# Kernel optimization log

Hardware: AMD Instinct MI355X
Metric: run time of the kernel (lower is better)

## Reference

```python
import jax, jax.numpy as jnp
import numpy as np


def _wn_dense_relu(x, v, g, bias):
    # torch weight_norm over dim=0: w[h,:] = g[h] * v[h,:] / ||v[h,:]||
    w = g[:, None] * v / jnp.linalg.norm(v, axis=1, keepdims=True)  # (hid, inp)
    return jax.nn.relu(jnp.einsum('bld,hd->blh', x, w) + bias)


def _masked_softmax(scores, mask, axis):
    # additive large-negative masking, numerically stable softmax
    return jax.nn.softmax(scores + jnp.where(mask > 0, 0.0, -1e9), axis=axis)


def setup_inputs() -> dict:
    key = jax.random.key(0)
    ks = jax.random.split(key, 6)
    B, La, Lb, D, H = 8, 2048, 2048, 256, 256
    return {
        'a': jax.random.normal(ks[0], (B, La, D), dtype=jnp.float32),
        'b': jax.random.normal(ks[1], (B, Lb, D), dtype=jnp.float32),
        'mask_a': jax.random.randint(ks[2], (B, La), 0, 2, dtype=jnp.int32),
        'mask_b': jax.random.randint(ks[3], (B, Lb), 0, 2, dtype=jnp.int32),
        'a_v': jax.random.normal(ks[4], (H, D), dtype=jnp.float32) * (2.0 / D) ** 0.5,
        'a_g': jnp.ones((H,), dtype=jnp.float32),
        'a_bias': jnp.zeros((H,), dtype=jnp.float32),
        'b_v': jax.random.normal(ks[5], (H, D), dtype=jnp.float32) * (2.0 / D) ** 0.5,
        'b_g': jnp.ones((H,), dtype=jnp.float32),
        'b_bias': jnp.zeros((H,), dtype=jnp.float32),
        'tau': jnp.asarray((1.0 / H) ** 0.5, dtype=jnp.float32),
    }


def reference(a, b, mask_a, mask_b, a_v, a_g, a_bias, b_v, b_g, b_bias, tau):
    ha = _wn_dense_relu(a, a_v, a_g, a_bias)                 # (B, La, H)
    hb = _wn_dense_relu(b, b_v, b_g, b_bias)                 # (B, Lb, H)
    attn = jnp.einsum('bih,bjh->bij', ha, hb) * tau          # (B, La, Lb)
    weight_a = _masked_softmax(attn, mask_a[:, :, None], axis=1)  # softmax over La
    weight_b = _masked_softmax(attn, mask_b[:, None, :], axis=2)  # softmax over Lb
    align_a = jnp.einsum('bij,bjd->bid', weight_b, b)        # (B, La, D)
    align_b = jnp.einsum('bij,bid->bjd', weight_a, a)        # (B, Lb, D)
    return align_a, align_b
```

## Files before the change

kernel.cpp:

```cpp
#include <hip/hip_runtime.h>
#include <hip/hip_bf16.h>
#include <stdint.h>

#define B_   8
#define L_   2048
#define D_   256
#define H_   256
#define TJ   64
#define NT   (L_/TJ)
#define BM   64
#define LOG2E 1.4426950408889634f

typedef short bf16x8 __attribute__((ext_vector_type(8)));
typedef short bf16x4 __attribute__((ext_vector_type(4)));
typedef unsigned short u16x4 __attribute__((ext_vector_type(4)));
typedef float f32x4  __attribute__((ext_vector_type(4)));

#define MFMA(a,b,c) __builtin_amdgcn_mfma_f32_16x16x32_bf16(a,b,c,0,0,0)
#define EX2(x) __builtin_amdgcn_exp2f(x)

typedef unsigned int u32;
__device__ __forceinline__ void gload_lds16(const void* g, void* l){
  __builtin_amdgcn_global_load_lds((const __attribute__((address_space(1))) u32*)g,
                                   (__attribute__((address_space(3))) u32*)l, 16, 0, 0);
}

__device__ __forceinline__ unsigned short f2bf(float f){
  __hip_bfloat16 h = __float2bfloat16(f);
  unsigned short us;
  __builtin_memcpy(&us, &h, 2);
  return us;
}
__device__ __forceinline__ float bf2f(unsigned short u){
  u32 t = ((u32)u) << 16;
  float f;
  __builtin_memcpy(&f, &t, 4);
  return f;
}

__device__ __forceinline__ void bar_lgkm(){
  asm volatile("s_waitcnt lgkmcnt(0)" ::: "memory");
  __builtin_amdgcn_s_barrier();
  __builtin_amdgcn_sched_barrier(0);
}
__device__ __forceinline__ void bar_all(){
  asm volatile("s_waitcnt vmcnt(0) lgkmcnt(0)" ::: "memory");
  __builtin_amdgcn_s_barrier();
  __builtin_amdgcn_sched_barrier(0);
}

__global__ __launch_bounds__(256) void wnorm_kernel(const float* __restrict__ av,
      const float* __restrict__ ag, const float* __restrict__ bv,
      const float* __restrict__ bg, unsigned short* __restrict__ wa,
      unsigned short* __restrict__ wb, float* __restrict__ maxn){
  int sel = blockIdx.y;
  if (blockIdx.x == 0 && threadIdx.x < 8) maxn[sel*8 + threadIdx.x] = 0.f;
  const float* v = sel ? bv : av;
  const float* g = sel ? bg : ag;
  unsigned short* w = sel ? wb : wa;
  int h = blockIdx.x;
  int d = threadIdx.x;
  float x = v[h*D_ + d];
  float sq = x*x;
  for (int off = 32; off; off >>= 1) sq += __shfl_down(sq, off, 64);
  __shared__ float red[4];
  int lane = threadIdx.x & 63, wid = threadIdx.x >> 6;
  if (lane == 0) red[wid] = sq;
  __syncthreads();
  float tot = red[0] + red[1] + red[2] + red[3];
  float scale = g[h] / sqrtf(tot);
  w[h*D_ + d] = f2bf(x * scale);
}

__global__ __launch_bounds__(256) void hgemm_kernel(const float* __restrict__ a,
      const float* __restrict__ b, const unsigned short* __restrict__ wa,
      const unsigned short* __restrict__ wb, const float* __restrict__ a_bias,
      const float* __restrict__ b_bias, const float* __restrict__ tau_ptr,
      unsigned short* __restrict__ ha, unsigned short* __restrict__ hb,
      unsigned short* __restrict__ aT, unsigned short* __restrict__ bT,
      float* __restrict__ rn_a, float* __restrict__ rn_b,
      float* __restrict__ maxn){
  __shared__ __align__(16) unsigned short xlk[64][256];
  __shared__ float redm[4];
  int sel = blockIdx.y;
  const float* x = sel ? b : a;
  const unsigned short* w = sel ? wb : wa;
  const float* bias = sel ? b_bias : a_bias;
  unsigned short* hx = sel ? hb : ha;
  unsigned short* xT = sel ? bT : aT;
  float* rn = sel ? rn_b : rn_a;
  float scale = sel ? 1.0f : tau_ptr[0] * LOG2E;
  int m0 = blockIdx.x * 64;
  int bz = m0 / L_, l0 = m0 % L_;
  int tid = threadIdx.x;
  int lane = tid & 63, wid = tid >> 6;
  int p = lane & 15, q = lane >> 4;

  {
    int r0 = tid >> 6;
    int c  = (tid & 63) * 4;
    int slot = c >> 3, half = (c >> 2) & 1;
    #pragma unroll
    for (int it = 0; it < 16; ++it){
      int row = it*4 + r0;
      f32x4 v = *(const f32x4*)(x + (size_t)(m0 + row) * 256 + c);
      uint2 wv;
      wv.x = (u32)f2bf(v[0]) | ((u32)f2bf(v[1]) << 16);
      wv.y = (u32)f2bf(v[2]) | ((u32)f2bf(v[3]) << 16);
      *(uint2*)((char*)&xlk[row][0] + ((slot ^ (row & 7)) << 4) + half*8) = wv;
    }
  }
  __syncthreads();

  bf16x8 af[8];
  {
    int row = wid*16 + p;
    #pragma unroll
    for (int kk = 0; kk < 8; ++kk)
      af[kk] = *(const bf16x8*)((char*)&xlk[row][0] + (((kk*4 + q) ^ (row & 7)) << 4));
  }
  f32x4 acc[16] = {};
  #pragma unroll
  for (int kk = 0; kk < 8; kk++){
    #pragma unroll
    for (int n = 0; n < 16; n++){
      bf16x8 bfr = *(const bf16x8*)(w + (size_t)(n*16 + p) * 256 + kk*32 + q*8);
      acc[n] = MFMA(af[kk], bfr, acc[n]);
    }
  }

  float rs[4] = {0.f, 0.f, 0.f, 0.f};
  #pragma unroll
  for (int n = 0; n < 16; n++){
    float bv = bias[n*16 + p];
    #pragma unroll
    for (int r = 0; r < 4; r++){
      int orow = m0 + wid*16 + q*4 + r;
      float vv = acc[n][r] + bv;
      vv = vv > 0.f ? vv : 0.f;
      float sv = vv * scale;
      rs[r] += sv * sv;
      hx[(size_t)orow * 256 + n*16 + p] = f2bf(sv);
    }
  }
  #pragma unroll
  for (int off = 1; off < 16; off <<= 1)
    #pragma unroll
    for (int r = 0; r < 4; r++)
      rs[r] += __shfl_xor(rs[r], off, 64);
  float lmax = 0.f;
  float rv[4];
  #pragma unroll
  for (int r = 0; r < 4; r++){
    rv[r] = sqrtf(rs[r]) * 1.01f;
    lmax = fmaxf(lmax, rv[r]);
  }
  if (p == 0){
    #pragma unroll
    for (int r = 0; r < 4; r++)
      rn[m0 + wid*16 + q*4 + r] = rv[r];
  }
  lmax = fmaxf(lmax, __shfl_xor(lmax, 16, 64));
  lmax = fmaxf(lmax, __shfl_xor(lmax, 32, 64));
  if (lane == 0) redm[wid] = lmax;
  __syncthreads();
  if (tid == 0){
    float bm = fmaxf(fmaxf(redm[0], redm[1]), fmaxf(redm[2], redm[3]));
    atomicMax((u32*)&maxn[sel*8 + bz], __float_as_uint(bm));
  }

  #pragma unroll
  for (int it = 0; it < 16; it++){
    int d = it*16 + (tid >> 4);
    int c = (tid & 15) * 4;
    bf16x4 v;
    #pragma unroll
    for (int j = 0; j < 4; j++){
      int row = c + j;
      v[j] = (short)*((const unsigned short*)((char*)&xlk[row][0]
                + (((d >> 3) ^ (row & 7)) << 4)) + (d & 7));
    }
    *(bf16x4*)(xT + ((size_t)bz*D_ + d)*L_ + l0 + c) = v;
  }
}

__global__ __launch_bounds__(256, 2) void flash_kernel(
    const unsigned short* __restrict__ ha, const unsigned short* __restrict__ hb,
    const unsigned short* __restrict__ aT, const unsigned short* __restrict__ bT,
    const int* __restrict__ mask_a, const int* __restrict__ mask_b,
    const float* __restrict__ rn_a, const float* __restrict__ rn_b,
    const float* __restrict__ maxn, float* __restrict__ out)
{
  __shared__ __align__(16) unsigned short HBT[64][256];
  __shared__ __align__(16) unsigned short VTL[256][64];
  __shared__ __align__(16) unsigned short WT[2][32][64];
  __shared__ unsigned short MSKB[2048];
  __shared__ float SST[4][32];

  const int bid = blockIdx.x;
  const int s   = bid & 15;
  const int dir = s >> 3;
  const int bz  = s & 7;
  const int i0  = (bid >> 4) * BM;
  const int tid = threadIdx.x;
  const int lane = tid & 63;
  const int wid  = tid >> 6;
  const int wr = wid >> 1, wc = wid & 1;
  const int p = lane & 15, q = lane >> 4;

  const unsigned short* hA = dir ? hb : ha;
  const unsigned short* hB = dir ? ha : hb;
  const unsigned short* vT = dir ? aT : bT;
  const int* mask = dir ? mask_a : mask_b;
  const float* rnA = dir ? rn_b : rn_a;
  const float mxB  = maxn[(dir ^ 1)*8 + bz];
  float* outp = out + ((size_t)dir * B_ + bz) * L_ * D_;

  const unsigned short* hAp = hA + (size_t)bz * L_ * H_;
  const unsigned short* hBp = hB + (size_t)bz * L_ * H_;
  const unsigned short* vTp = vT + (size_t)bz * D_ * L_;
  const int* mp = mask + bz * L_;

  const int hb_r0 = tid >> 5;
  const int hb_s  = tid & 31;
  const int vt_r0 = tid >> 3;
  const int vt_s  = tid & 7;

  bf16x8 af[2][8];
  #pragma unroll
  for (int g = 0; g < 2; ++g)
    #pragma unroll
    for (int kk = 0; kk < 8; ++kk)
      af[g][kk] = *(const bf16x8*)(hAp + (size_t)(i0 + wr*32 + g*16 + p) * H_ + kk*32 + q*8);

  float m_p[2];
  #pragma unroll
  for (int g = 0; g < 2; ++g)
    m_p[g] = rnA[bz*L_ + i0 + wr*32 + g*16 + p] * mxB;

  #pragma unroll
  for (int i = 0; i < 8; ++i){
    int idx = tid + i*256;
    MSKB[idx] = f2bf((mp[idx] > 0) ? 0.f : -1e9f);
  }

  f32x4 acc[2][8];
  #pragma unroll
  for (int g = 0; g < 2; ++g)
    #pragma unroll
    for (int n = 0; n < 8; ++n) acc[g][n] = (f32x4){0.f,0.f,0.f,0.f};
  float s_run[2];
  s_run[0] = s_run[1] = 0.f;

  #define STAGE_HB(jj0) do {                                                      \
    _Pragma("unroll")                                                             \
    for (int k = 0; k < 8; ++k){                                                  \
      int rr = k*8 + hb_r0;                                                       \
      int sp = hb_s ^ (rr & 7);                                                   \
      gload_lds16(hBp + (size_t)((jj0) + rr) * H_ + sp*8,                         \
                  &HBT[0][0] + k*2048 + tid*8);                                   \
    }                                                                             \
  } while(0)
  #define STAGE_VT(jj0) do {                                                      \
    _Pragma("unroll")                                                             \
    for (int k = 0; k < 8; ++k){                                                  \
      int rr = k*32 + vt_r0;                                                      \
      int sp = vt_s ^ (rr & 7);                                                   \
      gload_lds16(vTp + (size_t)rr * L_ + (jj0) + sp*8,                           \
                  &VTL[0][0] + k*2048 + tid*8);                                   \
    }                                                                             \
  } while(0)

  STAGE_HB(0);
  STAGE_VT(0);
  bar_all();

  for (int jt = 0; jt < NT; ++jt){
    const int j0 = jt * TJ;

    f32x4 accp[2][2];
    #pragma unroll
    for (int g = 0; g < 2; ++g)
      #pragma unroll
      for (int cg = 0; cg < 2; ++cg) accp[g][cg] = (f32x4){0.f,0.f,0.f,0.f};
    __builtin_amdgcn_s_setprio(1);
    #pragma unroll
    for (int kk = 0; kk < 8; ++kk){
      const int rb = wc*32 + p;
      const int sp = ((kk*4 + q) ^ (p & 7)) * 8;
      bf16x8 b0 = *(const bf16x8*)(&HBT[0][0] + rb*256 + sp);
      bf16x8 b1 = *(const bf16x8*)(&HBT[0][0] + (rb+16)*256 + sp);
      accp[0][0] = MFMA(b0, af[0][kk], accp[0][0]);
      accp[1][0] = MFMA(b0, af[1][kk], accp[1][0]);
      accp[0][1] = MFMA(b1, af[0][kk], accp[0][1]);
      accp[1][1] = MFMA(b1, af[1][kk], accp[1][1]);
    }
    __builtin_amdgcn_s_setprio(0);

    u16x4 k0 = *(const u16x4*)(&MSKB[j0 + wc*32 + q*4]);
    u16x4 k1 = *(const u16x4*)(&MSKB[j0 + wc*32 + 16 + q*4]);
    f32x4 mm0, mm1;
    #pragma unroll
    for (int r = 0; r < 4; ++r){ mm0[r] = bf2f(k0[r]); mm1[r] = bf2f(k1[r]); }

    #pragma unroll
    for (int g = 0; g < 2; ++g){
      #pragma unroll
      for (int cg = 0; cg < 2; ++cg){
        const f32x4 mm = cg ? mm1 : mm0;
        float w0 = EX2(accp[g][cg][0] + mm[0] - m_p[g]);
        float w1 = EX2(accp[g][cg][1] + mm[1] - m_p[g]);
        float w2 = EX2(accp[g][cg][2] + mm[2] - m_p[g]);
        float w3 = EX2(accp[g][cg][3] + mm[3] - m_p[g]);
        s_run[g] += (w0 + w1) + (w2 + w3);
        uint2 wv;
        wv.x = (u32)f2bf(w0) | ((u32)f2bf(w1) << 16);
        wv.y = (u32)f2bf(w2) | ((u32)f2bf(w3) << 16);
        int row = g*16 + p;
        int sl  = (wc*4 + cg*2 + (q>>1)) ^ (row & 7);
        *(uint2*)(&WT[wr][0][0] + row*64 + (sl<<3) + ((q&1)<<2)) = wv;
      }
    }
    bar_lgkm();

    if (jt + 1 < NT) STAGE_HB(j0 + TJ);

    bf16x8 wf[2][2];
    #pragma unroll
    for (int g = 0; g < 2; ++g)
      #pragma unroll
      for (int ks = 0; ks < 2; ++ks){
        int row = g*16 + p;
        wf[g][ks] = *(const bf16x8*)(&WT[wr][0][0] + row*64
                                     + ((((ks*4 + q) ^ (row & 7)))<<3));
      }

    __builtin_amdgcn_s_setprio(1);
    #pragma unroll
    for (int n = 0; n < 8; ++n){
      const int d = wc*128 + n*16 + p;
      #pragma unroll
      for (int ks = 0; ks < 2; ++ks){
        const int sp = ((ks*4 + q) ^ (d & 7)) * 8;
        bf16x8 vf = *(const bf16x8*)(&VTL[0][0] + d*64 + sp);
        acc[0][n] = MFMA(wf[0][ks], vf, acc[0][n]);
        acc[1][n] = MFMA(wf[1][ks], vf, acc[1][n]);
      }
    }
    __builtin_amdgcn_s_setprio(0);

    bar_all();
    if (jt + 1 < NT){
      STAGE_VT(j0 + TJ);
      bar_all();
    }
  }
  #undef STAGE_HB
  #undef STAGE_VT

  s_run[0] += __shfl_xor(s_run[0], 16, 64);
  s_run[0] += __shfl_xor(s_run[0], 32, 64);
  s_run[1] += __shfl_xor(s_run[1], 16, 64);
  s_run[1] += __shfl_xor(s_run[1], 32, 64);
  if (q == 0){
    SST[wid][p]      = s_run[0];
    SST[wid][16 + p] = s_run[1];
  }
  __syncthreads();
  float invS[2][4];
  #pragma unroll
  for (int g = 0; g < 2; ++g)
    #pragma unroll
    for (int r = 0; r < 4; ++r){
      int idx = g*16 + q*4 + r;
      invS[g][r] = 1.0f / (SST[wr*2][idx] + SST[wr*2 + 1][idx]);
    }

  #pragma unroll
  for (int g = 0; g < 2; ++g)
    #pragma unroll
    for (int n = 0; n < 8; ++n)
      #pragma unroll
      for (int r = 0; r < 4; ++r){
        int row = i0 + wr*32 + g*16 + q*4 + r;
        outp[(size_t)row * D_ + wc*128 + n*16 + p] = acc[g][n][r] * invS[g][r];
      }
}

extern "C" void kernel_launch(void* const* d_in, const int* in_sizes, int n_in,
                              void* d_out, int out_size, void* d_ws, size_t ws_size,
                              hipStream_t stream) {
  const float* a      = (const float*)d_in[0];
  const float* b      = (const float*)d_in[1];
  const int*   mask_a = (const int*)d_in[2];
  const int*   mask_b = (const int*)d_in[3];
  const float* a_v    = (const float*)d_in[4];
  const float* a_g    = (const float*)d_in[5];
  const float* a_bias = (const float*)d_in[6];
  const float* b_v    = (const float*)d_in[7];
  const float* b_g    = (const float*)d_in[8];
  const float* b_bias = (const float*)d_in[9];
  const float* tau    = (const float*)d_in[10];

  float* out = (float*)d_out;

  char* ws = (char*)d_ws;
  const size_t SZ_W  = (size_t)H_ * D_ * 2;
  const size_t SZ_H  = (size_t)B_ * L_ * H_ * 2;
  unsigned short* wa = (unsigned short*)(ws);
  unsigned short* wb = (unsigned short*)(ws + SZ_W);
  unsigned short* ha = (unsigned short*)(ws + 2*SZ_W);
  unsigned short* hb = (unsigned short*)(ws + 2*SZ_W + SZ_H);
  unsigned short* aT = (unsigned short*)(ws + 2*SZ_W + 2*SZ_H);
  unsigned short* bT = (unsigned short*)(ws + 2*SZ_W + 3*SZ_H);
  float* rn_a = (float*)(ws + 2*SZ_W + 4*SZ_H);
  float* rn_b = rn_a + (size_t)B_ * L_;
  float* maxn = rn_b + (size_t)B_ * L_;
  size_t need = 2*SZ_W + 4*SZ_H + 2*(size_t)B_*L_*4 + 64;
  if (ws_size < need) return;

  wnorm_kernel<<<dim3(H_, 2), 256, 0, stream>>>(a_v, a_g, b_v, b_g, wa, wb, maxn);

  {
    dim3 g((B_*L_)/64, 2);
    hgemm_kernel<<<g, 256, 0, stream>>>(a, b, wa, wb, a_bias, b_bias, tau,
                                        ha, hb, aT, bT, rn_a, rn_b, maxn);
  }

  {
    flash_kernel<<<dim3((L_/BM) * B_ * 2), 256, 0, stream>>>(
        ha, hb, aT, bT, mask_a, mask_b, rn_a, rn_b, maxn, out);
  }
}
```

Before: 133.1 us.

## Retile hgemm warps to 32x128 and stage outputs through LDS for coalesced stores

Each wave now computes two 16-row groups across half of the H columns, so every weight fragment loaded from global feeds two MFMAs, halving per-wave weight traffic. The bf16 results are written into the reused LDS tile and then copied out with 16-byte coalesced stores instead of scattered 2-byte global stores. Row norms are combined across the two column halves through a small LDS reduction, which adds two extra barriers.

After: 121.8 us (median of 2 runs). -8.5%, faster.

```diff
diff --git a/kernel.cpp b/kernel.cpp
--- a/kernel.cpp
+++ b/kernel.cpp
@@ -81,6 +81,7 @@
       float* __restrict__ rn_a, float* __restrict__ rn_b,
       float* __restrict__ maxn){
   __shared__ __align__(16) unsigned short xlk[64][256];
+  __shared__ float redp[2][2][32];
   __shared__ float redm[4];
   int sel = blockIdx.y;
   const float* x = sel ? b : a;
@@ -94,6 +95,7 @@
   int bz = m0 / L_, l0 = m0 % L_;
   int tid = threadIdx.x;
   int lane = tid & 63, wid = tid >> 6;
+  int rp = wid >> 1, ch = wid & 1;
   int p = lane & 15, q = lane >> 4;
 
   {
@@ -112,61 +114,27 @@
   }
   __syncthreads();
 
-  bf16x8 af[8];
-  {
-    int row = wid*16 + p;
+  bf16x8 af[2][8];
+  #pragma unroll
+  for (int g = 0; g < 2; ++g){
+    int row = rp*32 + g*16 + p;
     #pragma unroll
     for (int kk = 0; kk < 8; ++kk)
-      af[kk] = *(const bf16x8*)((char*)&xlk[row][0] + (((kk*4 + q) ^ (row & 7)) << 4));
-  }
-  f32x4 acc[16] = {};
+      af[g][kk] = *(const bf16x8*)((char*)&xlk[row][0] + (((kk*4 + q) ^ (row & 7)) << 4));
+  }
+  f32x4 acc[2][8];
+  #pragma unroll
+  for (int g = 0; g < 2; ++g)
+    #pragma unroll
+    for (int n = 0; n < 8; ++n) acc[g][n] = (f32x4){0.f,0.f,0.f,0.f};
   #pragma unroll
   for (int kk = 0; kk < 8; kk++){
     #pragma unroll
-    for (int n = 0; n < 16; n++){
-      bf16x8 bfr = *(const bf16x8*)(w + (size_t)(n*16 + p) * 256 + kk*32 + q*8);
-      acc[n] = MFMA(af[kk], bfr, acc[n]);
-    }
-  }
-
-  float rs[4] = {0.f, 0.f, 0.f, 0.f};
-  #pragma unroll
-  for (int n = 0; n < 16; n++){
-    float bv = bias[n*16 + p];
-    #pragma unroll
-    for (int r = 0; r < 4; r++){
-      int orow = m0 + wid*16 + q*4 + r;
-      float vv = acc[n][r] + bv;
-      vv = vv > 0.f ? vv : 0.f;
-      float sv = vv * scale;
-      rs[r] += sv * sv;
-      hx[(size_t)orow * 256 + n*16 + p] = f2bf(sv);
-    }
-  }
-  #pragma unroll
-  for (int off = 1; off < 16; off <<= 1)
-    #pragma unroll
-    for (int r = 0; r < 4; r++)
-      rs[r] += __shfl_xor(rs[r], off, 64);
-  float lmax = 0.f;
-  float rv[4];
-  #pragma unroll
-  for (int r = 0; r < 4; r++){
-    rv[r] = sqrtf(rs[r]) * 1.01f;
-    lmax = fmaxf(lmax, rv[r]);
-  }
-  if (p == 0){
-    #pragma unroll
-    for (int r = 0; r < 4; r++)
-      rn[m0 + wid*16 + q*4 + r] = rv[r];
-  }
-  lmax = fmaxf(lmax, __shfl_xor(lmax, 16, 64));
-  lmax = fmaxf(lmax, __shfl_xor(lmax, 32, 64));
-  if (lane == 0) redm[wid] = lmax;
-  __syncthreads();
-  if (tid == 0){
-    float bm = fmaxf(fmaxf(redm[0], redm[1]), fmaxf(redm[2], redm[3]));
-    atomicMax((u32*)&maxn[sel*8 + bz], __float_as_uint(bm));
+    for (int n = 0; n < 8; n++){
+      bf16x8 bfr = *(const bf16x8*)(w + (size_t)(ch*128 + n*16 + p) * 256 + kk*32 + q*8);
+      acc[0][n] = MFMA(af[0][kk], bfr, acc[0][n]);
+      acc[1][n] = MFMA(af[1][kk], bfr, acc[1][n]);
+    }
   }
 
   #pragma unroll
@@ -181,6 +149,67 @@
                 + (((d >> 3) ^ (row & 7)) << 4)) + (d & 7));
     }
     *(bf16x4*)(xT + ((size_t)bz*D_ + d)*L_ + l0 + c) = v;
+  }
+  __syncthreads();
+
+  unsigned short* hl = &xlk[0][0];
+  float rs[2][4] = {{0.f,0.f,0.f,0.f},{0.f,0.f,0.f,0.f}};
+  #pragma unroll
+  for (int g = 0; g < 2; ++g)
+    #pragma unroll
+    for (int n = 0; n < 8; ++n){
+      float bv = bias[ch*128 + n*16 + p];
+      #pragma unroll
+      for (int r = 0; r < 4; ++r){
+        int row = rp*32 + g*16 + q*4 + r;
+        float vv = acc[g][n][r] + bv;
+        vv = vv > 0.f ? vv : 0.f;
+        float sv = vv * scale;
+        rs[g][r] += sv * sv;
+        hl[row*256 + ch*128 + n*16 + p] = f2bf(sv);
+      }
+    }
+  #pragma unroll
+  for (int off = 1; off < 16; off <<= 1)
+    #pragma unroll
+    for (int g = 0; g < 2; ++g)
+      #pragma unroll
+      for (int r = 0; r < 4; r++)
+        rs[g][r] += __shfl_xor(rs[g][r], off, 64);
+  if (p == 0){
+    #pragma unroll
+    for (int g = 0; g < 2; ++g)
+      #pragma unroll
+      for (int r = 0; r < 4; ++r)
+        redp[ch][rp][g*16 + q*4 + r] = rs[g][r];
+  }
+  __syncthreads();
+
+  float lmax = 0.f;
+  #pragma unroll
+  for (int g = 0; g < 2; ++g)
+    #pragma unroll
+    for (int r = 0; r < 4; ++r){
+      int idx = g*16 + q*4 + r;
+      float tot = redp[0][rp][idx] + redp[1][rp][idx];
+      float rv = sqrtf(tot) * 1.01f;
+      lmax = fmaxf(lmax, rv);
+      if (ch == 0 && p == 0) rn[m0 + rp*32 + idx] = rv;
+    }
+  lmax = fmaxf(lmax, __shfl_xor(lmax, 16, 64));
+  lmax = fmaxf(lmax, __shfl_xor(lmax, 32, 64));
+  if (lane == 0) redm[wid] = lmax;
+
+  #pragma unroll
+  for (int i = 0; i < 8; ++i){
+    int idx = i*256 + tid;
+    bf16x8 hv = *(const bf16x8*)(hl + idx*8);
+    *(bf16x8*)(hx + (size_t)m0*256 + (size_t)idx*8) = hv;
+  }
+  __syncthreads();
+  if (tid == 0){
+    float bm = fmaxf(fmaxf(redm[0], redm[1]), fmaxf(redm[2], redm[3]));
+    atomicMax((u32*)&maxn[sel*8 + bz], __float_as_uint(bm));
   }
 }
 
```
